# Kernel optimization log

Hardware: AMD Instinct MI355X
Metric: run time of the kernel (lower is better)

The kernel has to match this reference:

```python
import jax, jax.numpy as jnp
import numpy as np

N = 100000   # nodes
E = 1600000  # edges (avg degree 16)
IN = 128     # in_feats
H = 4        # num_heads
D = 32       # out_feats per head
HD = H * D   # 128
LN_EPS = 1e-5


def setup_inputs() -> dict:
    key = jax.random.key(0)
    ks = jax.random.split(key, 16)
    w = lambda k, shp: (jax.random.normal(k, shp, dtype=jnp.float32) * 0.05)
    feat = jax.random.normal(ks[0], (N, IN), dtype=jnp.float32)
    src = jax.random.randint(ks[1], (E,), 0, N, dtype=jnp.int32)
    # ensure every destination node has >=1 incoming edge (no 0-in-degree)
    dst = jnp.concatenate([
        jnp.arange(N, dtype=jnp.int32),
        jax.random.randint(ks[2], (E - N,), 0, N, dtype=jnp.int32),
    ])
    return {
        "feat": feat, "src": src, "dst": dst,
        "Wq": w(ks[3], (IN, HD)), "bq": jnp.zeros((HD,), jnp.float32),
        "Wk": w(ks[4], (IN, HD)), "bk": jnp.zeros((HD,), jnp.float32),
        "Wv": w(ks[5], (IN, HD)), "bv": jnp.zeros((HD,), jnp.float32),
        "Wskip": w(ks[6], (IN, HD)), "bskip": jnp.zeros((HD,), jnp.float32),
        "Wgate": w(ks[7], (3 * HD, 1)), "bgate": jnp.zeros((1,), jnp.float32),
        "gamma": jnp.ones((HD,), jnp.float32), "beta": jnp.zeros((HD,), jnp.float32),
        "prelu_a": jnp.asarray(0.25, jnp.float32),
    }


def reference(feat, src, dst, Wq, bq, Wk, bk, Wv, bv, Wskip, bskip,
              Wgate, bgate, gamma, beta, prelu_a):
    n = feat.shape[0]
    q = (feat @ Wq + bq).reshape(n, H, D)   # src-side 'ft'
    k = (feat @ Wk + bk).reshape(n, H, D)   # dst-side 'ft'
    v = (feat @ Wv + bv).reshape(n, H, D)
    # edge scores: u_dot_v per head, scaled by 1/sqrt(D)
    a = jnp.einsum('ehd,ehd->eh', q[src], k[dst]) / jnp.sqrt(jnp.float32(D))  # [E,H]
    # edge_softmax: softmax over incoming edges of each destination node
    m = jax.ops.segment_max(a, dst, num_segments=n)          # [N,H]
    ex = jnp.exp(a - m[dst])                                  # [E,H]
    den = jax.ops.segment_sum(ex, dst, num_segments=n)        # [N,H]
    sa = ex / den[dst]                                        # [E,H]
    # weighted scatter-sum aggregation: sum_e sa * v[src] -> dst
    agg = jax.ops.segment_sum(sa[:, :, None] * v[src], dst, num_segments=n)
    rst = agg.reshape(n, HD)
    # skip connection + gate
    skip = feat @ Wskip + bskip
    g = jax.nn.sigmoid(jnp.concatenate([skip, rst, skip - rst], axis=-1) @ Wgate + bgate)
    rst = g * skip + (1.0 - g) * rst
    # layer norm
    mu = jnp.mean(rst, axis=-1, keepdims=True)
    var = jnp.mean(jnp.square(rst - mu), axis=-1, keepdims=True)
    rst = (rst - mu) * jax.lax.rsqrt(var + LN_EPS) * gamma + beta
    # PReLU (single shared slope)
    return jnp.where(rst > 0, rst, prelu_a * rst)
```

## Files before the change

kernel.cpp:

```cpp
#include <hip/hip_runtime.h>
#include <hip/hip_bf16.h>
#include <hip/hip_fp16.h>
#include <math.h>

#define N_NODES 100000
#define N_EDGES 1600000
#define NBUK 196
#define NSB  256
#define EPB  6250

typedef __attribute__((ext_vector_type(8))) short bf16x8;
typedef __attribute__((ext_vector_type(4))) float f32x4;
typedef __attribute__((ext_vector_type(2))) float f32x2;

__device__ __forceinline__ short f2bf_s(float x) {
    __hip_bfloat16 b = __float2bfloat16(x);
    return *reinterpret_cast<short*>(&b);
}
__device__ __forceinline__ __half2 bc2(unsigned u) {
    return *reinterpret_cast<__half2*>(&u);
}
__device__ __forceinline__ unsigned bcu(__half2 h) {
    return *reinterpret_cast<unsigned*>(&h);
}
__device__ __forceinline__ unsigned pack2h(float a, float b) {
    __half ha = __float2half(a), hb = __float2half(b);
    return (unsigned)*reinterpret_cast<unsigned short*>(&ha)
         | ((unsigned)*reinterpret_cast<unsigned short*>(&hb) << 16);
}

__global__ __launch_bounds__(256) void hist2_wt(
    const int* __restrict__ dst,
    const float* __restrict__ Wq, const float* __restrict__ Wk,
    const float* __restrict__ Wv, const float* __restrict__ Ws,
    int* __restrict__ histT, unsigned short* __restrict__ Wtb)
{
    int bid = blockIdx.x, tid = threadIdx.x;
    if (bid < NSB) {
        __shared__ int h[4 * NBUK];
        for (int t = tid; t < 4 * NBUK; t += 256) h[t] = 0;
        __syncthreads();
        int w = tid >> 6;
        for (int i = tid; i < EPB; i += 256)
            atomicAdd(&h[w * NBUK + (dst[bid * EPB + i] >> 9)], 1);
        __syncthreads();
        if (tid < NBUK)
            histT[tid * NSB + bid] = h[tid] + h[NBUK + tid]
                                   + h[2 * NBUK + tid] + h[3 * NBUK + tid];
    } else {
        int j = (bid - NSB) * 256 + tid;
        int j8  = j & 7;
        int lr  = (j >> 3) & 15;
        int cf  = (j >> 7) & 7;
        int lg  = (j >> 10) & 3;
        int kks = (j >> 12) & 3;
        int m   = j >> 14;
        int k   = kks * 32 + lg * 8 + j8;
        int col = cf * 16 + lr;
        const float* W = (m == 0) ? Wq : (m == 1) ? Wk : (m == 2) ? Wv : Ws;
        Wtb[j] = (unsigned short)f2bf_s(W[(size_t)k * 128 + col]);
    }
}

__global__ __launch_bounds__(256) void scan_block2(
    const int* __restrict__ in, int* __restrict__ outlocal, int* __restrict__ bsums)
{
    __shared__ int s[256];
    int i = blockIdx.x * 256 + threadIdx.x;
    int x = in[i];
    s[threadIdx.x] = x;
    __syncthreads();
    #pragma unroll
    for (int o = 1; o < 256; o <<= 1) {
        int t = (threadIdx.x >= o) ? s[threadIdx.x - o] : 0;
        __syncthreads();
        s[threadIdx.x] += t;
        __syncthreads();
    }
    outlocal[i] = s[threadIdx.x] - x;
    if (threadIdx.x == 255) bsums[blockIdx.x] = s[255];
}

__global__ __launch_bounds__(256) void scatter2(
    const int* __restrict__ src, const int* __restrict__ dst,
    const int* __restrict__ boffs, const int* __restrict__ bsums,
    unsigned* __restrict__ tmp)
{
    __shared__ int cur[NBUK];
    __shared__ int bsc[NBUK];
    __shared__ int s[256];
    int bid = blockIdx.x, tid = threadIdx.x;
    if (tid < NBUK) cur[tid] = 0;
    int x = (tid < NBUK) ? bsums[tid] : 0;
    s[tid] = x;
    __syncthreads();
    #pragma unroll
    for (int o = 1; o < 256; o <<= 1) {
        int t = (tid >= o) ? s[tid - o] : 0;
        __syncthreads();
        s[tid] += t;
        __syncthreads();
    }
    if (tid < NBUK) bsc[tid] = s[tid] - x;
    __syncthreads();

    for (int i = tid; i < EPB; i += 256) {
        int e = bid * EPB + i;
        int d = dst[e];
        int sv = src[e];
        int j = d >> 9;
        int r = atomicAdd(&cur[j], 1);
        int pos = boffs[j * NSB + bid] + bsc[j] + r;
        tmp[pos] = ((unsigned)(d & 511) << 17) | (unsigned)sv;
    }
}

__global__ __launch_bounds__(256) void bucket_sort(
    const unsigned* __restrict__ tmp, const int* __restrict__ bsums,
    int* __restrict__ sorted_src, int* __restrict__ offs)
{
    int bid = blockIdx.x, tid = threadIdx.x;

    __shared__ int h[512];
    __shared__ int o_[512];
    __shared__ int s_[256];
    __shared__ int baseSh;

    int x = (tid < NBUK) ? bsums[tid] : 0;
    s_[tid] = x;
    __syncthreads();
    #pragma unroll
    for (int o = 1; o < 256; o <<= 1) {
        int t = (tid >= o) ? s_[tid - o] : 0;
        __syncthreads();
        s_[tid] += t;
        __syncthreads();
    }
    if (tid == bid) baseSh = s_[tid] - x;
    h[tid] = 0; h[tid + 256] = 0;
    __syncthreads();
    int base = baseSh;
    int cnt  = bsums[bid];

    for (int i = tid; i < cnt; i += 256)
        atomicAdd(&h[tmp[base + i] >> 17], 1);
    __syncthreads();

    int a0 = h[2 * tid], a1 = h[2 * tid + 1];
    s_[tid] = a0 + a1;
    __syncthreads();
    #pragma unroll
    for (int o = 1; o < 256; o <<= 1) {
        int t = (tid >= o) ? s_[tid - o] : 0;
        __syncthreads();
        s_[tid] += t;
        __syncthreads();
    }
    int eb = s_[tid] - a0 - a1;
    o_[2 * tid] = eb;
    o_[2 * tid + 1] = eb + a0;
    __syncthreads();

    for (int t = tid; t < 512; t += 256) {
        int n = bid * 512 + t;
        if (n < N_NODES) offs[n] = base + o_[t];
    }
    __syncthreads();

    for (int i = tid; i < cnt; i += 256) {
        unsigned rec = tmp[base + i];
        int r = atomicAdd(&o_[rec >> 17], 1);
        sorted_src[base + r] = (int)((rec & 0x1FFFFu) << 7);
    }
}

__global__ __launch_bounds__(256) void gemm_mfma(
    const float* __restrict__ feat, const unsigned short* __restrict__ Wtb,
    const float* __restrict__ bq, const float* __restrict__ bk,
    const float* __restrict__ bv, const float* __restrict__ bs,
    unsigned char* __restrict__ q8, __half* __restrict__ vh,
    __half* __restrict__ ks_)
{
    __shared__ __align__(16) unsigned short Atile[32][136];
    __shared__ __align__(16) unsigned char  Oq8[32][144];
    __shared__ __align__(16) unsigned char  Ovh[32][272];
    __shared__ __align__(16) unsigned char  Oks[32][528];

    const int tid = threadIdx.x;
    const int r0  = blockIdx.x * 32;

    {
        int row = tid >> 3;
        int cg  = (tid & 7) * 16;
        const float4* fp = (const float4*)(feat + (size_t)(r0 + row) * 128 + cg);
        float4 f0 = fp[0], f1 = fp[1], f2 = fp[2], f3 = fp[3];
        unsigned short* ap = &Atile[row][cg];
        ap[0]  = (unsigned short)f2bf_s(f0.x); ap[1]  = (unsigned short)f2bf_s(f0.y);
        ap[2]  = (unsigned short)f2bf_s(f0.z); ap[3]  = (unsigned short)f2bf_s(f0.w);
        ap[4]  = (unsigned short)f2bf_s(f1.x); ap[5]  = (unsigned short)f2bf_s(f1.y);
        ap[6]  = (unsigned short)f2bf_s(f1.z); ap[7]  = (unsigned short)f2bf_s(f1.w);
        ap[8]  = (unsigned short)f2bf_s(f2.x); ap[9]  = (unsigned short)f2bf_s(f2.y);
        ap[10] = (unsigned short)f2bf_s(f2.z); ap[11] = (unsigned short)f2bf_s(f2.w);
        ap[12] = (unsigned short)f2bf_s(f3.x); ap[13] = (unsigned short)f2bf_s(f3.y);
        ap[14] = (unsigned short)f2bf_s(f3.z); ap[15] = (unsigned short)f2bf_s(f3.w);
    }
    __syncthreads();

    const int mat = tid >> 6;
    const int l   = tid & 63;
    const int lr  = l & 15;
    const int lg  = l >> 4;
    const float* bias = (mat == 0) ? bq : (mat == 1) ? bk : (mat == 2) ? bv : bs;

    f32x4 acc[2][8];
    #pragma unroll
    for (int i = 0; i < 2; i++)
        #pragma unroll
        for (int j = 0; j < 8; j++) acc[i][j] = (f32x4){0.f, 0.f, 0.f, 0.f};

    const unsigned short* wb = Wtb + (size_t)mat * 16384 + lg * 1024 + lr * 8;

    #pragma unroll
    for (int kks = 0; kks < 4; kks++) {
        const int k0 = kks * 32 + lg * 8;
        bf16x8 a[2], b[8];
        #pragma unroll
        for (int rf = 0; rf < 2; rf++)
            a[rf] = *(const bf16x8*)&Atile[rf * 16 + lr][k0];
        #pragma unroll
        for (int cf = 0; cf < 8; cf++)
            b[cf] = *(const bf16x8*)(wb + kks * 4096 + cf * 128);
        #pragma unroll
        for (int rf = 0; rf < 2; rf++)
            #pragma unroll
            for (int cf = 0; cf < 8; cf++)
                acc[rf][cf] = __builtin_amdgcn_mfma_f32_16x16x32_bf16(
                    b[cf], a[rf], acc[rf][cf], 0, 0, 0);
    }

    #pragma unroll
    for (int rf = 0; rf < 2; rf++) {
        int rl = rf * 16 + lr;
        #pragma unroll
        for (int cf = 0; cf < 8; cf++) {
            int colb = cf * 16 + lg * 4;
            float4 b4 = *(const float4*)(bias + colb);
            float a0 = acc[rf][cf][0] + b4.x, a1 = acc[rf][cf][1] + b4.y;
            float a2 = acc[rf][cf][2] + b4.z, a3 = acc[rf][cf][3] + b4.w;
            if (mat == 0) {
                unsigned u = (unsigned)__builtin_amdgcn_cvt_pk_fp8_f32(a0, a1, 0, false);
                u = (unsigned)__builtin_amdgcn_cvt_pk_fp8_f32(a2, a3, (int)u, true);
                *(unsigned*)&Oq8[rl][colb] = u;
            } else if (mat == 2) {
                uint2 pk; pk.x = pack2h(a0, a1); pk.y = pack2h(a2, a3);
                *(uint2*)&Ovh[rl][colb * 2] = pk;
            } else {
                uint2 pk; pk.x = pack2h(a0, a1); pk.y = pack2h(a2, a3);
                *(uint2*)&Oks[rl][((mat == 3) ? 256 : 0) + colb * 2] = pk;
            }
        }
    }
    __syncthreads();

    {
        int row = tid >> 3;
        int c16 = (tid & 7) * 16;
        *(uint4*)(q8 + (size_t)(r0 + row) * 128 + c16) = *(const uint4*)&Oq8[row][c16];
        {
            char* gp = (char*)vh + (size_t)(r0 + row) * 256 + (tid & 7) * 32;
            const char* lp = (const char*)&Ovh[row][0] + (tid & 7) * 32;
            ((uint4*)gp)[0] = ((const uint4*)lp)[0];
            ((uint4*)gp)[1] = ((const uint4*)lp)[1];
        }
        {
            char* gp = (char*)ks_ + (size_t)(r0 + row) * 512 + (tid & 7) * 64;
            const char* lp = (const char*)&Oks[row][0] + (tid & 7) * 64;
            ((uint4*)gp)[0] = ((const uint4*)lp)[0];
            ((uint4*)gp)[1] = ((const uint4*)lp)[1];
            ((uint4*)gp)[2] = ((const uint4*)lp)[2];
            ((uint4*)gp)[3] = ((const uint4*)lp)[3];
        }
    }
}

__global__ __launch_bounds__(256) void node_fused(
    const unsigned char* __restrict__ q8, const __half* __restrict__ vh,
    const __half* __restrict__ ks_,
    const int* __restrict__ offs, const int* __restrict__ sorted_src,
    const float* __restrict__ wg, const float* __restrict__ bg,
    const float* __restrict__ gamma, const float* __restrict__ beta,
    const float* __restrict__ pa, float* __restrict__ out)
{
    int wid = threadIdx.x >> 6;
    int l   = threadIdx.x & 63;
    int qtr = l >> 4;
    int c   = l & 15;
    int n = blockIdx.x * 4 + wid;
    if (n >= N_NODES) return;

    int start = offs[n];
    int end   = (n + 1 < N_NODES) ? offs[n + 1] : N_EDGES;

    const uint4* krow = (const uint4*)ks_;
    uint4 kp  = krow[(size_t)n * 32 + c];
    uint4 sp4 = krow[(size_t)n * 32 + 16 + c];

    f32x2 kp0, kp1, kp2, kp3;
    {
        __half2 h;
        h = bc2(kp.x); kp0 = (f32x2){__low2float(h), __high2float(h)};
        h = bc2(kp.y); kp1 = (f32x2){__low2float(h), __high2float(h)};
        h = bc2(kp.z); kp2 = (f32x2){__low2float(h), __high2float(h)};
        h = bc2(kp.w); kp3 = (f32x2){__low2float(h), __high2float(h)};
    }

    float den = 0.f;
    __half2 ag0 = bc2(0u), ag1 = bc2(0u), ag2 = bc2(0u), ag3 = bc2(0u);
    const float C = 0.25503483f;

    const char* qb = (const char*)q8 + c * 8;
    const char* vb = (const char*)vh + c * 16;

    int base = start;
    int sA = sorted_src[min(base + qtr, end - 1)];
    uint2 qA = *(const uint2*)(qb + sA);
    uint4 vA = *(const uint4*)(vb + 2 * (size_t)sA);
    bool hasB = (base + 4) < end;
    uint2 qB; uint4 vB;
    if (hasB) {
        int sB = sorted_src[min(base + 4 + qtr, end - 1)];
        qB = *(const uint2*)(qb + sB);
        vB = *(const uint4*)(vb + 2 * (size_t)sB);
    }
    int sC = ((base + 8) < end) ? sorted_src[min(base + 8 + qtr, end - 1)] : 0;

    for (;;) {
        bool hasC = (base + 8) < end;
        uint2 qC; uint4 vC;
        if (hasC) {
            qC = *(const uint2*)(qb + sC);
            vC = *(const uint4*)(vb + 2 * (size_t)sC);
        }
        int sD = ((base + 12) < end) ? sorted_src[min(base + 12 + qtr, end - 1)] : 0;

        f32x2 q01 = __builtin_amdgcn_cvt_pk_f32_fp8((int)qA.x, false);
        f32x2 q23 = __builtin_amdgcn_cvt_pk_f32_fp8((int)qA.x, true);
        f32x2 q45 = __builtin_amdgcn_cvt_pk_f32_fp8((int)qA.y, false);
        f32x2 q67 = __builtin_amdgcn_cvt_pk_f32_fp8((int)qA.y, true);
        f32x2 d2 = q01 * kp0 + q23 * kp1 + q45 * kp2 + q67 * kp3;
        float d = d2[0] + d2[1];
        d += __shfl_xor(d, 1);
        d += __shfl_xor(d, 2);
        float e = (base + qtr < end) ? __builtin_amdgcn_exp2f(d * C) : 0.f;
        den += e;
        __half2 e2 = __float2half2_rn(e);
        ag0 = __hfma2(e2, bc2(vA.x), ag0);
        ag1 = __hfma2(e2, bc2(vA.y), ag1);
        ag2 = __hfma2(e2, bc2(vA.z), ag2);
        ag3 = __hfma2(e2, bc2(vA.w), ag3);

        if (!hasB) break;
        base += 4;
        qA = qB; vA = vB; qB = qC; vB = vC; sC = sD; hasB = hasC;
    }

    den += __shfl_xor(den, 16);
    den += __shfl_xor(den, 32);
    ag0 = __hadd2(ag0, bc2(__shfl_xor(bcu(ag0), 16)));
    ag1 = __hadd2(ag1, bc2(__shfl_xor(bcu(ag1), 16)));
    ag2 = __hadd2(ag2, bc2(__shfl_xor(bcu(ag2), 16)));
    ag3 = __hadd2(ag3, bc2(__shfl_xor(bcu(ag3), 16)));
    ag0 = __hadd2(ag0, bc2(__shfl_xor(bcu(ag0), 32)));
    ag1 = __hadd2(ag1, bc2(__shfl_xor(bcu(ag1), 32)));
    ag2 = __hadd2(ag2, bc2(__shfl_xor(bcu(ag2), 32)));
    ag3 = __hadd2(ag3, bc2(__shfl_xor(bcu(ag3), 32)));

    float rd = 1.f / den;
    float r[8];
    r[0] = __low2float(ag0) * rd; r[1] = __high2float(ag0) * rd;
    r[2] = __low2float(ag1) * rd; r[3] = __high2float(ag1) * rd;
    r[4] = __low2float(ag2) * rd; r[5] = __high2float(ag2) * rd;
    r[6] = __low2float(ag3) * rd; r[7] = __high2float(ag3) * rd;

    float s[8];
    s[0] = __low2float(bc2(sp4.x)); s[1] = __high2float(bc2(sp4.x));
    s[2] = __low2float(bc2(sp4.y)); s[3] = __high2float(bc2(sp4.y));
    s[4] = __low2float(bc2(sp4.z)); s[5] = __high2float(bc2(sp4.z));
    s[6] = __low2float(bc2(sp4.w)); s[7] = __high2float(bc2(sp4.w));

    const float4* wgf = (const float4*)wg;
    float4 w0a = wgf[2 * c],      w0b = wgf[2 * c + 1];
    float4 w1a = wgf[32 + 2 * c], w1b = wgf[32 + 2 * c + 1];
    float4 w2a = wgf[64 + 2 * c], w2b = wgf[64 + 2 * c + 1];
    float w0[8] = {w0a.x, w0a.y, w0a.z, w0a.w, w0b.x, w0b.y, w0b.z, w0b.w};
    float w1[8] = {w1a.x, w1a.y, w1a.z, w1a.w, w1b.x, w1b.y, w1b.z, w1b.w};
    float w2[8] = {w2a.x, w2a.y, w2a.z, w2a.w, w2b.x, w2b.y, w2b.z, w2b.w};

    float gs = 0.f;
    #pragma unroll
    for (int j = 0; j < 8; j++)
        gs += s[j] * w0[j] + r[j] * w1[j] + (s[j] - r[j]) * w2[j];
    gs += __shfl_xor(gs, 1);
    gs += __shfl_xor(gs, 2);
    gs += __shfl_xor(gs, 4);
    gs += __shfl_xor(gs, 8);
    float g = 1.f / (1.f + __builtin_amdgcn_exp2f(-(gs + bg[0]) * 1.4426950408889634f));

    #pragma unroll
    for (int j = 0; j < 8; j++) r[j] = g * s[j] + (1.f - g) * r[j];

    float mu = 0.f;
    #pragma unroll
    for (int j = 0; j < 8; j++) mu += r[j];
    mu += __shfl_xor(mu, 1);
    mu += __shfl_xor(mu, 2);
    mu += __shfl_xor(mu, 4);
    mu += __shfl_xor(mu, 8);
    mu *= (1.f / 128.f);

    float var = 0.f;
    #pragma unroll
    for (int j = 0; j < 8; j++) { float e0 = r[j] - mu; var += e0 * e0; }
    var += __shfl_xor(var, 1);
    var += __shfl_xor(var, 2);
    var += __shfl_xor(var, 4);
    var += __shfl_xor(var, 8);
    var *= (1.f / 128.f);
    float inv = rsqrtf(var + 1e-5f);

    if (qtr == 0) {
        float4 ga = ((const float4*)gamma)[2 * c], gb = ((const float4*)gamma)[2 * c + 1];
        float4 ba = ((const float4*)beta)[2 * c],  bb = ((const float4*)beta)[2 * c + 1];
        float gm[8] = {ga.x, ga.y, ga.z, ga.w, gb.x, gb.y, gb.z, gb.w};
        float bt[8] = {ba.x, ba.y, ba.z, ba.w, bb.x, bb.y, bb.z, bb.w};
        float al = pa[0];
        float y[8];
        #pragma unroll
        for (int j = 0; j < 8; j++) {
            float t = (r[j] - mu) * inv * gm[j] + bt[j];
            y[j] = (t > 0.f) ? t : al * t;
        }
        float4* op = (float4*)(out + (size_t)n * 128 + c * 8);
        op[0] = (float4){y[0], y[1], y[2], y[3]};
        op[1] = (float4){y[4], y[5], y[6], y[7]};
    }
}

extern "C" void kernel_launch(void* const* d_in, const int* in_sizes, int n_in,
                              void* d_out, int out_size, void* d_ws, size_t ws_size,
                              hipStream_t stream) {
    const float* feat  = (const float*)d_in[0];
    const int*   src   = (const int*)d_in[1];
    const int*   dst   = (const int*)d_in[2];
    const float* Wq    = (const float*)d_in[3];
    const float* bq    = (const float*)d_in[4];
    const float* Wk    = (const float*)d_in[5];
    const float* bk    = (const float*)d_in[6];
    const float* Wv    = (const float*)d_in[7];
    const float* bv    = (const float*)d_in[8];
    const float* Wsk   = (const float*)d_in[9];
    const float* bsk   = (const float*)d_in[10];
    const float* Wg    = (const float*)d_in[11];
    const float* bg    = (const float*)d_in[12];
    const float* gamma = (const float*)d_in[13];
    const float* beta  = (const float*)d_in[14];
    const float* pa    = (const float*)d_in[15];
    float* out = (float*)d_out;

    char* p = (char*)d_ws;
    unsigned char* q8  = (unsigned char*)p;  p += (size_t)N_NODES * 128;
    __half*        vh  = (__half*)p;         p += (size_t)N_NODES * 128 * 2;
    __half*        ks_ = (__half*)p;         p += (size_t)N_NODES * 256 * 2;
    unsigned short* Wtb = (unsigned short*)p;  p += (size_t)4 * 128 * 128 * 2;
    int*      sorted_src = (int*)p;      p += (size_t)N_EDGES * 4;
    unsigned* tmp        = (unsigned*)p; p += (size_t)N_EDGES * 4;
    int*      histT      = (int*)p;      p += (size_t)NBUK * NSB * 4;
    int*      boffs      = (int*)p;      p += (size_t)NBUK * NSB * 4;
    int*      offs       = (int*)p;      p += (size_t)N_NODES * 4;
    int*      bsums      = (int*)p;      p += 4096;

    hist2_wt<<<NSB + 256, 256, 0, stream>>>(dst, Wq, Wk, Wv, Wsk, histT, Wtb);
    scan_block2<<<NBUK, 256, 0, stream>>>(histT, boffs, bsums);
    scatter2<<<NSB, 256, 0, stream>>>(src, dst, boffs, bsums, tmp);
    bucket_sort<<<NBUK, 256, 0, stream>>>(tmp, bsums, sorted_src, offs);
    gemm_mfma<<<3125, 256, 0, stream>>>(feat, Wtb, bq, bk, bv, bsk, q8, vh, ks_);
    node_fused<<<(N_NODES + 3) / 4, 256, 0, stream>>>(q8, vh, ks_, offs, sorted_src,
                                                      Wg, bg, gamma, beta, pa, out);
}
```

Measured before the change: 205.8 us.

## Fuse bucket sort into GEMM kernel as extra blocks sharing LDS union

Merges the bucket_sort kernel into the projection GEMM launch by appending NBUK extra blocks that run the sort path, and overlays the GEMM A tile, the K/skip output tile and the sort scratch in one shared-memory union. The aim is to remove one kernel launch and let the independent sort work overlap with the GEMM. The union adds a barrier between the MFMA loop and the epilogue writes. The sort blocks are scheduled after the 3125 GEMM blocks, so they may end up as a tail rather than overlapping.

Result: faster. 200.1 us (median of 2 runs) (-2.7%).

```diff
diff --git a/kernel.cpp b/kernel.cpp
--- a/kernel.cpp
+++ b/kernel.cpp
@@ -8,6 +8,7 @@
 #define NBUK 196
 #define NSB  256
 #define EPB  6250
+#define GEMM_BLOCKS 3125
 
 typedef __attribute__((ext_vector_type(8))) short bf16x8;
 typedef __attribute__((ext_vector_type(4))) float f32x4;
@@ -115,86 +116,84 @@
     }
 }
 
-__global__ __launch_bounds__(256) void bucket_sort(
-    const unsigned* __restrict__ tmp, const int* __restrict__ bsums,
-    int* __restrict__ sorted_src, int* __restrict__ offs)
-{
-    int bid = blockIdx.x, tid = threadIdx.x;
-
-    __shared__ int h[512];
-    __shared__ int o_[512];
-    __shared__ int s_[256];
-    __shared__ int baseSh;
-
-    int x = (tid < NBUK) ? bsums[tid] : 0;
-    s_[tid] = x;
-    __syncthreads();
-    #pragma unroll
-    for (int o = 1; o < 256; o <<= 1) {
-        int t = (tid >= o) ? s_[tid - o] : 0;
-        __syncthreads();
-        s_[tid] += t;
-        __syncthreads();
-    }
-    if (tid == bid) baseSh = s_[tid] - x;
-    h[tid] = 0; h[tid + 256] = 0;
-    __syncthreads();
-    int base = baseSh;
-    int cnt  = bsums[bid];
-
-    for (int i = tid; i < cnt; i += 256)
-        atomicAdd(&h[tmp[base + i] >> 17], 1);
-    __syncthreads();
-
-    int a0 = h[2 * tid], a1 = h[2 * tid + 1];
-    s_[tid] = a0 + a1;
-    __syncthreads();
-    #pragma unroll
-    for (int o = 1; o < 256; o <<= 1) {
-        int t = (tid >= o) ? s_[tid - o] : 0;
-        __syncthreads();
-        s_[tid] += t;
-        __syncthreads();
-    }
-    int eb = s_[tid] - a0 - a1;
-    o_[2 * tid] = eb;
-    o_[2 * tid + 1] = eb + a0;
-    __syncthreads();
-
-    for (int t = tid; t < 512; t += 256) {
-        int n = bid * 512 + t;
-        if (n < N_NODES) offs[n] = base + o_[t];
-    }
-    __syncthreads();
-
-    for (int i = tid; i < cnt; i += 256) {
-        unsigned rec = tmp[base + i];
-        int r = atomicAdd(&o_[rec >> 17], 1);
-        sorted_src[base + r] = (int)((rec & 0x1FFFFu) << 7);
-    }
-}
-
-__global__ __launch_bounds__(256) void gemm_mfma(
+__global__ __launch_bounds__(256) void gemm_sort(
     const float* __restrict__ feat, const unsigned short* __restrict__ Wtb,
     const float* __restrict__ bq, const float* __restrict__ bk,
     const float* __restrict__ bv, const float* __restrict__ bs,
     unsigned char* __restrict__ q8, __half* __restrict__ vh,
-    __half* __restrict__ ks_)
+    __half* __restrict__ ks_,
+    const unsigned* __restrict__ tmp, const int* __restrict__ bsums,
+    int* __restrict__ sorted_src, int* __restrict__ offs)
 {
-    __shared__ __align__(16) unsigned short Atile[32][136];
-    __shared__ __align__(16) unsigned char  Oq8[32][144];
-    __shared__ __align__(16) unsigned char  Ovh[32][272];
-    __shared__ __align__(16) unsigned char  Oks[32][528];
+    __shared__ __align__(16) union {
+        unsigned short Atile[32][136];
+        unsigned char  Oks[32][528];
+        struct { int h[512]; int o_[512]; int s_[256]; int baseSh; } srt;
+    } U;
+    __shared__ __align__(16) unsigned char Oq8[32][144];
+    __shared__ __align__(16) unsigned char Ovh[32][272];
 
     const int tid = threadIdx.x;
-    const int r0  = blockIdx.x * 32;
+
+    if (blockIdx.x >= GEMM_BLOCKS) {
+        int bid = blockIdx.x - GEMM_BLOCKS;
+        int x = (tid < NBUK) ? bsums[tid] : 0;
+        U.srt.s_[tid] = x;
+        __syncthreads();
+        #pragma unroll
+        for (int o = 1; o < 256; o <<= 1) {
+            int t = (tid >= o) ? U.srt.s_[tid - o] : 0;
+            __syncthreads();
+            U.srt.s_[tid] += t;
+            __syncthreads();
+        }
+        if (tid == bid) U.srt.baseSh = U.srt.s_[tid] - x;
+        U.srt.h[tid] = 0; U.srt.h[tid + 256] = 0;
+        __syncthreads();
+        int base = U.srt.baseSh;
+        int cnt  = bsums[bid];
+
+        for (int i = tid; i < cnt; i += 256)
+            atomicAdd(&U.srt.h[tmp[base + i] >> 17], 1);
+        __syncthreads();
+
+        int a0 = U.srt.h[2 * tid], a1 = U.srt.h[2 * tid + 1];
+        U.srt.s_[tid] = a0 + a1;
+        __syncthreads();
+        #pragma unroll
+        for (int o = 1; o < 256; o <<= 1) {
+            int t = (tid >= o) ? U.srt.s_[tid - o] : 0;
+            __syncthreads();
+            U.srt.s_[tid] += t;
+            __syncthreads();
+        }
+        int eb = U.srt.s_[tid] - a0 - a1;
+        U.srt.o_[2 * tid] = eb;
+        U.srt.o_[2 * tid + 1] = eb + a0;
+        __syncthreads();
+
+        for (int t = tid; t < 512; t += 256) {
+            int n = bid * 512 + t;
+            if (n < N_NODES) offs[n] = base + U.srt.o_[t];
+        }
+        __syncthreads();
+
+        for (int i = tid; i < cnt; i += 256) {
+            unsigned rec = tmp[base + i];
+            int r = atomicAdd(&U.srt.o_[rec >> 17], 1);
+            sorted_src[base + r] = (int)((rec & 0x1FFFFu) << 7);
+        }
+        return;
+    }
+
+    const int r0 = blockIdx.x * 32;
 
     {
         int row = tid >> 3;
         int cg  = (tid & 7) * 16;
         const float4* fp = (const float4*)(feat + (size_t)(r0 + row) * 128 + cg);
         float4 f0 = fp[0], f1 = fp[1], f2 = fp[2], f3 = fp[3];
-        unsigned short* ap = &Atile[row][cg];
+        unsigned short* ap = &U.Atile[row][cg];
         ap[0]  = (unsigned short)f2bf_s(f0.x); ap[1]  = (unsigned short)f2bf_s(f0.y);
         ap[2]  = (unsigned short)f2bf_s(f0.z); ap[3]  = (unsigned short)f2bf_s(f0.w);
         ap[4]  = (unsigned short)f2bf_s(f1.x); ap[5]  = (unsigned short)f2bf_s(f1.y);
@@ -226,7 +225,7 @@
         bf16x8 a[2], b[8];
         #pragma unroll
         for (int rf = 0; rf < 2; rf++)
-            a[rf] = *(const bf16x8*)&Atile[rf * 16 + lr][k0];
+            a[rf] = *(const bf16x8*)&U.Atile[rf * 16 + lr][k0];
         #pragma unroll
         for (int cf = 0; cf < 8; cf++)
             b[cf] = *(const bf16x8*)(wb + kks * 4096 + cf * 128);
@@ -237,6 +236,8 @@
                 acc[rf][cf] = __builtin_amdgcn_mfma_f32_16x16x32_bf16(
                     b[cf], a[rf], acc[rf][cf], 0, 0, 0);
     }
+
+    __syncthreads();
 
     #pragma unroll
     for (int rf = 0; rf < 2; rf++) {
@@ -256,7 +257,7 @@
                 *(uint2*)&Ovh[rl][colb * 2] = pk;
             } else {
                 uint2 pk; pk.x = pack2h(a0, a1); pk.y = pack2h(a2, a3);
-                *(uint2*)&Oks[rl][((mat == 3) ? 256 : 0) + colb * 2] = pk;
+                *(uint2*)&U.Oks[rl][((mat == 3) ? 256 : 0) + colb * 2] = pk;
             }
         }
     }
@@ -274,7 +275,7 @@
         }
         {
             char* gp = (char*)ks_ + (size_t)(r0 + row) * 512 + (tid & 7) * 64;
-            const char* lp = (const char*)&Oks[row][0] + (tid & 7) * 64;
+            const char* lp = (const char*)&U.Oks[row][0] + (tid & 7) * 64;
             ((uint4*)gp)[0] = ((const uint4*)lp)[0];
             ((uint4*)gp)[1] = ((const uint4*)lp)[1];
             ((uint4*)gp)[2] = ((const uint4*)lp)[2];
@@ -482,8 +483,9 @@
     hist2_wt<<<NSB + 256, 256, 0, stream>>>(dst, Wq, Wk, Wv, Wsk, histT, Wtb);
     scan_block2<<<NBUK, 256, 0, stream>>>(histT, boffs, bsums);
     scatter2<<<NSB, 256, 0, stream>>>(src, dst, boffs, bsums, tmp);
-    bucket_sort<<<NBUK, 256, 0, stream>>>(tmp, bsums, sorted_src, offs);
-    gemm_mfma<<<3125, 256, 0, stream>>>(feat, Wtb, bq, bk, bv, bsk, q8, vh, ks_);
+    gemm_sort<<<GEMM_BLOCKS + NBUK, 256, 0, stream>>>(feat, Wtb, bq, bk, bv, bsk,
+                                                      q8, vh, ks_,
+                                                      tmp, bsums, sorted_src, offs);
     node_fused<<<(N_NODES + 3) / 4, 256, 0, stream>>>(q8, vh, ks_, offs, sorted_src,
                                                       Wg, bg, gamma, beta, pa, out);
 }
```
